# Kernel optimization log

Measured on AMD Instinct MI355X. Metric: run time of the kernel, lower is better.

The kernel has to match this reference:

```python
import jax, jax.numpy as jnp
import numpy as np

EPS = 1e-5

def setup_inputs() -> dict:
    key = jax.random.key(0)
    k1, k2, k3 = jax.random.split(key, 3)
    B, T, D, K = 8, 4096, 256, 2048
    x = jax.random.normal(k1, (B, T, D), dtype=jnp.float32)
    embedding_sum = jax.random.normal(k2, (K, D), dtype=jnp.float32)
    cluster_usage = jax.random.uniform(k3, (K,), dtype=jnp.float32)
    return {"x": x, "embedding_sum": embedding_sum, "cluster_usage": cluster_usage}

def reference(x, embedding_sum, cluster_usage):
    # embedding = embedding_sum / clamp(cluster_usage, eps)  -> [K, D]
    emb = embedding_sum / jnp.clip(cluster_usage, EPS, None)[:, None]
    shape = x.shape
    flat = x.reshape(-1, shape[-1])  # [N, D]
    # squared Euclidean distances (argmin-equivalent to torch.cdist p=2)
    d = (
        jnp.sum(flat * flat, axis=-1, keepdims=True)
        - 2.0 * flat @ emb.T
        + jnp.sum(emb * emb, axis=-1)
    )  # [N, K]
    flat_codes = jnp.argmin(d, axis=-1)  # [N]
    codes = flat_codes.reshape(shape[:-1])  # [B, T]
    quantized = emb[codes]  # [B, T, D]
    return quantized, codes
```

## Files before the change

kernel.cpp:

```cpp
#include <hip/hip_runtime.h>


#define EPSV 1e-5f
#define TAU  0.4f
#define DDIM 256
#define BM   128
#define BCL  128
#define NPART 2
#define NCT  8
#define RPB  8
#define KSPL 4
#define NROWS 32768
#define EB   32

typedef __attribute__((ext_vector_type(8))) _Float16 f16x8;
typedef __attribute__((ext_vector_type(4))) float f32x4;
typedef unsigned short u16;
typedef unsigned u32;
typedef unsigned long long u64;

__device__ __forceinline__ u16 f2h(float f) {
    f = fminf(fmaxf(f, -60000.f), 60000.f);
    const _Float16 h = (_Float16)f;
    return __builtin_bit_cast(u16, h);
}
__device__ __forceinline__ u32 umn(u32 a, u32 b) { return a < b ? a : b; }
__device__ __forceinline__ u32 umx(u32 a, u32 b) { return a > b ? a : b; }
__device__ __forceinline__ float unsort(u32 u) {
    const u32 v = (u & 0x80000000u) ? (u & 0x7FFFFFFFu) : ~u;
    return __builtin_bit_cast(float, v);
}
__device__ __forceinline__ u64 packdk(float d, int k) {
    u32 u = __builtin_bit_cast(u32, d);
    u = (u & 0x80000000u) ? ~u : (u | 0x80000000u);
    return ((u64)u << 32) | (u32)k;
}
__device__ __forceinline__ u32 pk2(float a, float b) {
    return (u32)f2h(a) | ((u32)f2h(b) << 16);
}

__global__ void prep(const float* __restrict__ esum,
                     const float* __restrict__ usage,
                     float* __restrict__ emb_t,
                     u16* __restrict__ eh,
                     float* __restrict__ enorm2,
                     int* __restrict__ counter,
                     int K) {
    const int b = blockIdx.x;
    if (b == 0 && threadIdx.x == 0) *counter = 0;
    __shared__ float tile[EB][DDIM + 1];
    const int k0 = b * EB;
    const int d  = threadIdx.x;
    for (int r = 0; r < EB; ++r) {
        const int k = k0 + r;
        const float u = fmaxf(usage[k], EPSV);
        const float e = esum[(size_t)k * DDIM + d] / u;
        tile[r][d] = e;
        eh[(size_t)k * DDIM + d] = f2h(e);
    }
    __syncthreads();
    if (threadIdx.x < EB) {
        const int r = threadIdx.x;
        float s = 0.f;
        #pragma unroll 8
        for (int dd = 0; dd < DDIM; ++dd) {
            const float e = tile[r][dd];
            s = fmaf(e, e, s);
        }
        enorm2[k0 + r] = s;
    }
    for (int it = 0; it < DDIM / 8; ++it) {
        const int dd   = it * 8 + (threadIdx.x >> 5);
        const int lane = threadIdx.x & 31;
        emb_t[(size_t)dd * K + k0 + lane] = tile[lane][dd];
    }
}

__global__ __launch_bounds__(256, 2) void vq_mfma(
        const float* __restrict__ x, const u16* __restrict__ eh,
        const float* __restrict__ enorm2,
        u32* __restrict__ pp1, u32* __restrict__ pp2, int N) {
    __shared__ __align__(16) u16 Als[BM * DDIM];
    __shared__ __align__(16) u16 Bls[BCL * 64];

    const int tid = threadIdx.x;
    const int l   = tid & 63;
    const int w   = tid >> 6;
    const int wr  = w >> 1, wc = w & 1;

    const int nwg = (N / BM) * NPART;
    const int q   = nwg >> 3;
    const int pb  = blockIdx.x;
    const int logical = (pb & 7) * q + (pb >> 3);
    const int rowblk  = logical >> 1;
    const int part    = logical & 1;
    const int n0      = rowblk * BM;
    const int cbase   = part * 1024;

    #pragma unroll
    for (int j = 0; j < 16; ++j) {
        const int slot = j * 256 + tid;
        const int row  = slot >> 5;
        const int c    = slot & 31;
        const int gc   = (c & 24) | ((c & 7) ^ (row & 7));
        const float* xp = x + (size_t)(n0 + row) * DDIM + gc * 8;
        const float4 v0 = *(const float4*)xp;
        const float4 v1 = *(const float4*)(xp + 4);
        uint4 hv;
        hv.x = pk2(v0.x, v0.y);
        hv.y = pk2(v0.z, v0.w);
        hv.z = pk2(v1.x, v1.y);
        hv.w = pk2(v1.z, v1.w);
        *(uint4*)((char*)Als + slot * 16) = hv;
    }

    u32 m1p[4][4], m2p[4][4];
    #pragma unroll
    for (int a = 0; a < 4; ++a)
        #pragma unroll
        for (int b = 0; b < 4; ++b) { m1p[a][b] = 0xFFFFFFFFu; m2p[a][b] = 0xFFFFFFFFu; }

    const int sgc = (l & 7) ^ ((l >> 3) & 7);

    __syncthreads();

    for (int ct = 0; ct < NCT; ++ct) {
        const int c0 = cbase + ct * BCL;
        f32x4 acc[4][4];
        #pragma unroll
        for (int a = 0; a < 4; ++a)
            #pragma unroll
            for (int b = 0; b < 4; ++b) acc[a][b] = (f32x4){0.f, 0.f, 0.f, 0.f};

        for (int ch = 0; ch < 4; ++ch) {
            const int colof = ch * 64;

            __syncthreads();
            #pragma unroll
            for (int j = 0; j < 4; ++j) {
                const int r = (w * 4 + j) * 8 + (l >> 3);
                const u16* gb = eh + (size_t)(c0 + r) * DDIM + colof + sgc * 8;
                __builtin_amdgcn_global_load_lds(
                    (const __attribute__((address_space(1))) void*)gb,
                    (__attribute__((address_space(3))) void*)((char*)Bls + (w * 4 + j) * 1024),
                    16, 0, 0);
            }
            __syncthreads();

            #pragma unroll
            for (int ks = 0; ks < 2; ++ks) {
                f16x8 af[4], bfr[4];
                #pragma unroll
                for (int f = 0; f < 4; ++f) {
                    const int arow   = wr * 64 + f * 16 + (l & 15);
                    const int achunk = ch * 8 + (((ks * 4 + (l >> 4))) ^ (l & 7));
                    af[f] = *(const f16x8*)((const char*)Als + arow * 512 + achunk * 16);
                    const int brow = wc * 64 + f * 16 + (l & 15);
                    const int bc   = (ks * 4 + (l >> 4)) ^ (l & 7);
                    bfr[f] = *(const f16x8*)((const char*)Bls + brow * 128 + bc * 16);
                }
                #pragma unroll
                for (int fm = 0; fm < 4; ++fm)
                    #pragma unroll
                    for (int fn = 0; fn < 4; ++fn)
                        acc[fm][fn] = __builtin_amdgcn_mfma_f32_16x16x32_f16(
                            af[fm], bfr[fn], acc[fm][fn], 0, 0, 0);
            }
        }

        #pragma unroll
        for (int fn = 0; fn < 4; ++fn) {
            const int k = c0 + wc * 64 + fn * 16 + (l & 15);
            const float en = enorm2[k];
            #pragma unroll
            for (int fm = 0; fm < 4; ++fm)
                #pragma unroll
                for (int i = 0; i < 4; ++i) {
                    const float s = fmaf(-2.0f, acc[fm][fn][i], en);
                    u32 u = __builtin_bit_cast(u32, s);
                    u = ((int)u < 0) ? ~u : (u | 0x80000000u);
                    const u32 p = (u & 0xFFFFF800u) | (u32)k;
                    m2p[fm][i] = umn(m2p[fm][i], umx(p, m1p[fm][i]));
                    m1p[fm][i] = umn(m1p[fm][i], p);
                }
        }
    }

    #pragma unroll
    for (int fm = 0; fm < 4; ++fm)
        #pragma unroll
        for (int i = 0; i < 4; ++i) {
            u32 p1 = m1p[fm][i], p2 = m2p[fm][i];
            #pragma unroll
            for (int mask = 1; mask < 16; mask <<= 1) {
                const u32 o1 = (u32)__shfl_xor((int)p1, mask, 64);
                const u32 o2 = (u32)__shfl_xor((int)p2, mask, 64);
                p2 = umn(umn(p2, o2), umx(p1, o1));
                p1 = umn(p1, o1);
            }
            m1p[fm][i] = p1; m2p[fm][i] = p2;
        }

    __syncthreads();
    u32* S1 = (u32*)Bls;
    u32* S2 = (u32*)((char*)Bls + 512);
    if (wc == 0 && (l & 15) == 0) {
        #pragma unroll
        for (int fm = 0; fm < 4; ++fm)
            #pragma unroll
            for (int i = 0; i < 4; ++i) {
                const int r = wr * 64 + fm * 16 + (l >> 4) * 4 + i;
                S1[r] = m1p[fm][i]; S2[r] = m2p[fm][i];
            }
    }
    __syncthreads();
    if (wc == 1 && (l & 15) == 0) {
        #pragma unroll
        for (int fm = 0; fm < 4; ++fm)
            #pragma unroll
            for (int i = 0; i < 4; ++i) {
                const int r = wr * 64 + fm * 16 + (l >> 4) * 4 + i;
                const u32 o1 = S1[r], o2 = S2[r];
                u32 p1 = m1p[fm][i], p2 = m2p[fm][i];
                const u32 M2 = umn(umn(p2, o2), umx(p1, o1));
                const u32 M1 = umn(p1, o1);
                const int n = n0 + r;
                pp1[(size_t)part * N + n] = M1;
                pp2[(size_t)part * N + n] = M2;
            }
    }
}

__global__ void combine(const u32* __restrict__ pp1, const u32* __restrict__ pp2,
                        int* __restrict__ codes_i, int* __restrict__ flags,
                        int* __restrict__ list, int* __restrict__ counter,
                        u64* __restrict__ packed, int N) {
    const int n = blockIdx.x * 256 + threadIdx.x;
    u32 p1 = pp1[n], p2 = pp2[n];
    #pragma unroll
    for (int j = 1; j < NPART; ++j) {
        const u32 o1 = pp1[(size_t)j * N + n], o2 = pp2[(size_t)j * N + n];
        p2 = umn(umn(p2, o2), umx(p1, o1));
        p1 = umn(p1, o1);
    }
    codes_i[n] = (int)(p1 & 0x7FFu);
    const float m1f = unsort(p1 & 0xFFFFF800u);
    const float m2f = unsort(p2 & 0xFFFFF800u);
    const int fl = (m2f - m1f < TAU) ? 1 : 0;
    flags[n] = fl;
    if (fl) {
        packed[n] = 0xFFFFFFFFFFFFFFFFull;
        const int idx = atomicAdd(counter, 1);
        list[idx] = n;
    }
}

__global__ __launch_bounds__(256) void rescue_c(
        const float* __restrict__ x, const float* __restrict__ emb_t,
        const float* __restrict__ enorm2,
        const int* __restrict__ list, const int* __restrict__ counter,
        u64* __restrict__ packed, int K) {
    __shared__ float xs[RPB][DDIM];
    const int t = threadIdx.x;
    const int l = t & 63;
    int cnt = *counter;
    cnt = cnt < 0 ? 0 : (cnt > NROWS ? NROWS : cnt);
    if (cnt == 0) return;
    const int nblk  = (cnt + RPB - 1) / RPB;
    const int items = nblk * KSPL;
    const int kc    = K / KSPL;

    for (int wi = blockIdx.x; wi < items; wi += gridDim.x) {
        const int g = wi >> 2;
        const int q = wi & 3;
        const int base = g * RPB;
        int rows[RPB];
        #pragma unroll
        for (int r = 0; r < RPB; ++r) {
            int idx = base + r;
            rows[r] = list[idx < cnt ? idx : cnt - 1];
        }
        __syncthreads();
        #pragma unroll
        for (int r = 0; r < RPB; ++r)
            xs[r][t] = x[(size_t)rows[r] * DDIM + t];
        __syncthreads();

        float acc[RPB][2];
        #pragma unroll
        for (int r = 0; r < RPB; ++r) { acc[r][0] = 0.f; acc[r][1] = 0.f; }

        const float* eb = emb_t + q * kc + 2 * t;
        #pragma unroll 8
        for (int d = 0; d < DDIM; ++d) {
            const float2 e = *(const float2*)&eb[(size_t)d * K];
            #pragma unroll
            for (int r = 0; r < RPB; ++r) {
                const float xv = xs[r][d];
                acc[r][0] = fmaf(xv, e.x, acc[r][0]);
                acc[r][1] = fmaf(xv, e.y, acc[r][1]);
            }
        }

        const int k0 = q * kc + 2 * t;
        const float en0 = enorm2[k0], en1 = enorm2[k0 + 1];
        #pragma unroll
        for (int r = 0; r < RPB; ++r) {
            const float s0 = fmaf(-2.0f, acc[r][0], en0);
            const float s1 = fmaf(-2.0f, acc[r][1], en1);
            float bd = s0; int bk = k0;
            if (s1 < bd) { bd = s1; bk = k0 + 1; }
            #pragma unroll
            for (int m = 1; m < 64; m <<= 1) {
                const float od = __shfl_xor(bd, m, 64);
                const int   ok = __shfl_xor(bk, m, 64);
                if (od < bd || (od == bd && ok < bk)) { bd = od; bk = ok; }
            }
            if (l == 0) atomicMin(&packed[rows[r]], packdk(bd, bk));
        }
    }
}

__global__ void gather_q(const float* __restrict__ esum,
                         const float* __restrict__ usage,
                         const int* __restrict__ codes_i,
                         const int* __restrict__ flags,
                         const u64* __restrict__ packed,
                         float* __restrict__ qout,
                         float* __restrict__ codes_f) {
    const int n = blockIdx.x * 4 + (threadIdx.x >> 6);
    const int c = threadIdx.x & 63;
    int k = codes_i[n];
    if (flags[n]) k = (int)(packed[n] & 0xFFFFFFFFull);
    if (c == 0) codes_f[n] = (float)k;
    const float u = fmaxf(usage[k], EPSV);
    float4 v = *(const float4*)&esum[(size_t)k * DDIM + c * 4];
    v.x /= u; v.y /= u; v.z /= u; v.w /= u;
    *(float4*)&qout[(size_t)n * DDIM + c * 4] = v;
}

extern "C" void kernel_launch(void* const* d_in, const int* in_sizes, int n_in,
                              void* d_out, int out_size, void* d_ws, size_t ws_size,
                              hipStream_t stream) {
    const float* x     = (const float*)d_in[0];
    const float* esum  = (const float*)d_in[1];
    const float* usage = (const float*)d_in[2];
    const int K = in_sizes[2];
    const int N = in_sizes[0] / DDIM;

    char* p = (char*)d_ws;
    u64*   packed  = (u64*)p;                  p += (size_t)N * 8;
    float* emb_t   = (float*)p;                p += (size_t)K * DDIM * 4;
    float* enorm2  = (float*)p;                p += (size_t)K * 4;
    u32*   pp1     = (u32*)p;                  p += (size_t)NPART * N * 4;
    u32*   pp2     = (u32*)p;                  p += (size_t)NPART * N * 4;
    int*   codes_i = (int*)p;                  p += (size_t)N * 4;
    int*   flags   = (int*)p;                  p += (size_t)N * 4;
    int*   list    = (int*)p;                  p += (size_t)N * 4;
    int*   counter = (int*)p;                  p += 256;
    u16*   eh      = (u16*)p;                  p += (size_t)K * DDIM * 2;

    float* qout    = (float*)d_out;
    float* codes_f = qout + (size_t)N * DDIM;

    prep<<<K / EB, 256, 0, stream>>>(esum, usage, emb_t, eh, enorm2, counter, K);
    vq_mfma<<<(N / BM) * NPART, 256, 0, stream>>>(x, eh, enorm2, pp1, pp2, N);
    combine<<<N / 256, 256, 0, stream>>>(pp1, pp2, codes_i, flags,
                                         list, counter, packed, N);
    rescue_c<<<1024, 256, 0, stream>>>(x, emb_t, enorm2, list, counter, packed, K);
    gather_q<<<N / 4, 256, 0, stream>>>(esum, usage, codes_i, flags, packed,
                                        qout, codes_f);
}
```

Baseline: 101.2 us.

## Prefetch codebook tiles into registers to overlap global loads with MFMA

Replaces the direct global-to-LDS loads of each 64-column codebook chunk with register prefetching. The next chunk is fetched into registers while the current chunk's MFMAs run, then written to the single LDS buffer between two barriers. The first chunk is issued before the x tile conversion so its latency is hidden there too. This is meant to hide global load latency that the old load-then-barrier sequence exposed, at the cost of 16 extra VGPRs per thread and separate LDS store instructions.

New measurement: 102.5 us. Within noise of the previous version (+1.3%).

```diff
diff --git a/kernel.cpp b/kernel.cpp
--- a/kernel.cpp
+++ b/kernel.cpp
@@ -97,6 +97,27 @@
     const int n0      = rowblk * BM;
     const int cbase   = part * 1024;
 
+    const int sgc = (l & 7) ^ ((l >> 3) & 7);
+
+    uint4 breg0, breg1, breg2, breg3;
+    auto issueB = [&](int rr) {
+        const int c0_    = cbase + (rr >> 2) * BCL;
+        const int colof_ = (rr & 3) * 64;
+        const u16* bbase = eh + colof_ + sgc * 8;
+        breg0 = *(const uint4*)(bbase + (size_t)(c0_ + (w * 4 + 0) * 8 + (l >> 3)) * DDIM);
+        breg1 = *(const uint4*)(bbase + (size_t)(c0_ + (w * 4 + 1) * 8 + (l >> 3)) * DDIM);
+        breg2 = *(const uint4*)(bbase + (size_t)(c0_ + (w * 4 + 2) * 8 + (l >> 3)) * DDIM);
+        breg3 = *(const uint4*)(bbase + (size_t)(c0_ + (w * 4 + 3) * 8 + (l >> 3)) * DDIM);
+    };
+    auto writeB = [&]() {
+        *(uint4*)((char*)Bls + (w * 4 + 0) * 1024 + l * 16) = breg0;
+        *(uint4*)((char*)Bls + (w * 4 + 1) * 1024 + l * 16) = breg1;
+        *(uint4*)((char*)Bls + (w * 4 + 2) * 1024 + l * 16) = breg2;
+        *(uint4*)((char*)Bls + (w * 4 + 3) * 1024 + l * 16) = breg3;
+    };
+
+    issueB(0);
+
     #pragma unroll
     for (int j = 0; j < 16; ++j) {
         const int slot = j * 256 + tid;
@@ -120,10 +141,10 @@
         #pragma unroll
         for (int b = 0; b < 4; ++b) { m1p[a][b] = 0xFFFFFFFFu; m2p[a][b] = 0xFFFFFFFFu; }
 
-    const int sgc = (l & 7) ^ ((l >> 3) & 7);
-
+    writeB();
     __syncthreads();
 
+    int rr = 0;
     for (int ct = 0; ct < NCT; ++ct) {
         const int c0 = cbase + ct * BCL;
         f32x4 acc[4][4];
@@ -132,20 +153,8 @@
             #pragma unroll
             for (int b = 0; b < 4; ++b) acc[a][b] = (f32x4){0.f, 0.f, 0.f, 0.f};
 
-        for (int ch = 0; ch < 4; ++ch) {
-            const int colof = ch * 64;
-
-            __syncthreads();
-            #pragma unroll
-            for (int j = 0; j < 4; ++j) {
-                const int r = (w * 4 + j) * 8 + (l >> 3);
-                const u16* gb = eh + (size_t)(c0 + r) * DDIM + colof + sgc * 8;
-                __builtin_amdgcn_global_load_lds(
-                    (const __attribute__((address_space(1))) void*)gb,
-                    (__attribute__((address_space(3))) void*)((char*)Bls + (w * 4 + j) * 1024),
-                    16, 0, 0);
-            }
-            __syncthreads();
+        for (int ch = 0; ch < 4; ++ch, ++rr) {
+            if (rr + 1 < NCT * 4) issueB(rr + 1);
 
             #pragma unroll
             for (int ks = 0; ks < 2; ++ks) {
@@ -166,6 +175,11 @@
                         acc[fm][fn] = __builtin_amdgcn_mfma_f32_16x16x32_f16(
                             af[fm], bfr[fn], acc[fm][fn], 0, 0, 0);
             }
+            __syncthreads();
+            if (rr + 1 < NCT * 4) {
+                writeB();
+            }
+            __syncthreads();
         }
 
         #pragma unroll
```
